# Optimization experiments

Measured on AMD Instinct MI355X. Metric: run time of the kernel, lower is better.

Reference implementation:

```python
import jax, jax.numpy as jnp
import numpy as np

N, E, VD, HD, ES = 10000, 80000, 32, 64, 68
NET_IN = VD * VD + 2 * HD + ES   # 1220: f2s(1024) + s[e0](64) + s[e1](64) + edge_s(68)
SELF_IN = VD * VD + 2 * HD       # 1152: temp_f2s(1024) + s(64) + s_c(64)
OUT_D = VD * VD + HD             # 1088: vector channel mixer + scalar update


def _lecun(k, fin, fout):
    return jax.random.normal(k, (fin, fout), jnp.float32) / jnp.sqrt(jnp.float32(fin))


def setup_inputs() -> dict:
    ks = jax.random.split(jax.random.key(0), 16)
    return {
        "f": jax.random.normal(ks[0], (N, 3, VD), jnp.float32),
        "s": jax.random.normal(ks[1], (N, HD), jnp.float32),
        "edge_f": jax.random.normal(ks[2], (E, 3, 1), jnp.float32),
        "edge_s": jax.random.normal(ks[3], (E, ES), jnp.float32),
        "W_emb1": _lecun(ks[4], 2 * VD + 1, VD),
        "net_W1": _lecun(ks[5], NET_IN, HD), "net_b1": jnp.zeros((HD,), jnp.float32),
        "net_W2": _lecun(ks[6], HD, HD), "net_b2": jnp.zeros((HD,), jnp.float32),
        "net_W3": _lecun(ks[7], HD, OUT_D), "net_b3": jnp.zeros((OUT_D,), jnp.float32),
        "W_emb2": _lecun(ks[8], 2 * VD, VD),
        "self_W1": _lecun(ks[9], SELF_IN, HD), "self_b1": jnp.zeros((HD,), jnp.float32),
        "self_W2": _lecun(ks[10], HD, HD), "self_b2": jnp.zeros((HD,), jnp.float32),
        "self_W3": _lecun(ks[11], HD, OUT_D), "self_b3": jnp.zeros((OUT_D,), jnp.float32),
        "edge_index": jax.random.randint(ks[12], (2, E), 0, N),
    }


def _mlp(x, W1, b1, W2, b2, W3, b3):
    h = jax.nn.relu(x @ W1 + b1)
    h = jax.nn.relu(h @ W2 + b2)
    return h @ W3 + b3


def _segment_mean(x, ids, n):
    tot = jax.ops.segment_sum(x, ids, num_segments=n)
    cnt = jax.ops.segment_sum(jnp.ones(ids.shape, x.dtype), ids, num_segments=n)
    return tot / jnp.maximum(cnt, 1.0).reshape((n,) + (1,) * (x.ndim - 1))


def _forward(f, s, edge_f, edge_s,
             W_emb1, net_W1, net_b1, net_W2, net_b2, net_W3, net_b3,
             W_emb2, self_W1, self_b1, self_W2, self_b2, self_W3, self_b3,
             edge_index):
    n = f.shape[0]
    e0, e1 = edge_index[0], edge_index[1]
    # --- edge message: gather -> embed -> gram einsum -> MLP ---
    _f = jnp.concatenate((f[e0], f[e1], edge_f), axis=-1)          # [E,3,2VD+1]
    _s = jnp.concatenate((s[e0], s[e1], edge_s), axis=-1)          # [E,2HD+ES]
    _f = _f @ W_emb1                                               # [E,3,VD]
    f2s = jnp.einsum('eij,eik->ejk', _f, _f).reshape(-1, VD * VD)  # _f^T @ _f, [E,VD*VD]
    Fn = jnp.linalg.norm(f2s, axis=-1, keepdims=True) + 1.0
    c = _mlp(jnp.concatenate((f2s, _s), axis=-1),
             net_W1, net_b1, net_W2, net_b2, net_W3, net_b3) / Fn  # [E,OUT_D]
    f_c = jnp.einsum('eij,ejk->eik', _f, c[:, :VD * VD].reshape(-1, VD, VD))  # [E,3,VD]
    f_c = _segment_mean(f_c, e0, n)                                # [N,3,VD]
    s_c = _segment_mean(c[:, VD * VD:], e0, n)                     # [N,HD]
    # --- node self-update ---
    tf = jnp.concatenate((f, f_c), axis=-1) @ W_emb2               # [N,3,VD]
    tf2s = jnp.einsum('nij,nik->njk', tf, tf).reshape(n, VD * VD)
    Fn2 = jnp.linalg.norm(tf2s, axis=-1, keepdims=True) + 1.0
    c2 = _mlp(jnp.concatenate((tf2s, s, s_c), axis=-1),
              self_W1, self_b1, self_W2, self_b2, self_W3, self_b3) / Fn2
    f_out = jnp.einsum('nij,njk->nik', tf, c2[:, :VD * VD].reshape(-1, VD, VD)) + f
    s_out = c2[:, VD * VD:] + s
    return f_out, s_out


def reference(f, s, edge_f, edge_s,
              W_emb1, net_W1, net_b1, net_W2, net_b2, net_W3, net_b3,
              W_emb2, self_W1, self_b1, self_W2, self_b2, self_W3, self_b3,
              edge_index):
    return _forward(f, s, edge_f, edge_s,
                    W_emb1, net_W1, net_b1, net_W2, net_b2, net_W3, net_b3,
                    W_emb2, self_W1, self_b1, self_W2, self_b2, self_W3, self_b3,
                    edge_index)
```

## Files before the change

kernel.cpp:

```cpp
#include <hip/hip_runtime.h>
#include <math.h>

#define NN 10000
#define NE 80000
#define SF 98
#define SFF 97
#define STX 72
#define NTRI 528
#define SAE 104
#define SAN 72

typedef __attribute__((ext_vector_type(8))) __bf16 bf16x8;
typedef __attribute__((ext_vector_type(8))) short short8v;
typedef __attribute__((ext_vector_type(4))) float f32x4;
typedef __attribute__((ext_vector_type(4))) unsigned uint4v;

__device__ __forceinline__ ushort f2bf(float x) {
  union { float f; unsigned u; } v; v.f = x;
  unsigned r = v.u + 0x7FFFu + ((v.u >> 16) & 1u);
  return (ushort)(r >> 16);
}
__device__ __forceinline__ void tri_ab(int k, int& a, int& b) {
  int aa = 0, rem = k;
  while (rem >= 32 - aa) { rem -= 32 - aa; ++aa; }
  a = aa; b = aa + rem;
}

__global__ __launch_bounds__(256)
void sgnn_hist(const int* __restrict__ eidx, int* __restrict__ deg) {
  const int e = blockIdx.x * 256 + threadIdx.x;
  if (e < NE) atomicAdd(deg + eidx[e], 1);
}

__global__ __launch_bounds__(1024)
void sgnn_scan(const int* __restrict__ deg, int* __restrict__ cursor,
               int* __restrict__ start) {
  __shared__ int sm[1024];
  __shared__ int carry;
  const int t = threadIdx.x;
  if (t == 0) carry = 0;
  __syncthreads();
  for (int base = 0; base < NN; base += 1024) {
    const int i = base + t;
    const int v = (i < NN) ? deg[i] : 0;
    sm[t] = v;
    __syncthreads();
    #pragma unroll
    for (int d = 1; d < 1024; d <<= 1) {
      const int add = (t >= d) ? sm[t - d] : 0;
      __syncthreads();
      sm[t] += add;
      __syncthreads();
    }
    const int excl = carry + sm[t] - v;
    if (i < NN) { cursor[i] = excl; start[i] = excl; }
    __syncthreads();
    if (t == 1023) carry += sm[1023];
    __syncthreads();
  }
}

__global__ __launch_bounds__(256)
void sgnn_scatter(const int* __restrict__ eidx, int* __restrict__ cursor,
                  int* __restrict__ sorted) {
  const int e = blockIdx.x * 256 + threadIdx.x;
  if (e < NE) {
    const int p = atomicAdd(cursor + eidx[e], 1);
    sorted[p] = e;
  }
}

__global__ __launch_bounds__(256)
void sgnn_wconv(const float* __restrict__ nW1, const float* __restrict__ nW2,
                const float* __restrict__ nW3, const float* __restrict__ sW1,
                const float* __restrict__ sW2, const float* __restrict__ sW3,
                const float* __restrict__ Wemb1, const float* __restrict__ Wemb2,
                ushort* __restrict__ wout, ushort* __restrict__ tab) {
  const int gid = blockIdx.x * 256 + threadIdx.x;
  if (gid >= 61 * 4096) {
    const int k = gid - 61 * 4096;
    if (k < NTRI) {
      int a, b; tri_ab(k, a, b);
      tab[k] = (ushort)(a | (b << 8) | ((a != b) ? 0x8000 : 0));
    }
    return;
  }
  const int tile = gid >> 12, idx = gid & 4095;
  const int c = idx >> 6, k = idx & 63;
  float v = 0.f;
  if (tile < 12) {
    const int T = tile;
    if (T < 8 || (T == 8 && k < 16)) {
      const int ktri = T * 64 + k;
      if (ktri < NTRI) {
        int a, b; tri_ab(ktri, a, b);
        v = nW1[(a * 32 + b) * 64 + c];
        if (a != b) v += nW1[(b * 32 + a) * 64 + c];
      }
    } else if (T == 8) { if (k < 20) v = nW1[(1216 + (k - 16)) * 64 + c]; }
    else if (T == 9)   v = nW1[(1024 + k) * 64 + c];
    else if (T == 10)  v = nW1[(1088 + k) * 64 + c];
    else               v = nW1[(1152 + k) * 64 + c];
  } else if (tile == 12) v = nW2[k * 64 + c];
  else if (tile < 30)    v = nW3[k * 1088 + (tile - 13) * 64 + c];
  else if (tile < 41) {
    const int T = tile - 30;
    if (T < 8 || (T == 8 && k < 16)) {
      const int ktri = T * 64 + k;
      if (ktri < NTRI) {
        int a, b; tri_ab(ktri, a, b);
        v = sW1[(a * 32 + b) * 64 + c];
        if (a != b) v += sW1[(b * 32 + a) * 64 + c];
      }
    } else if (T == 9) v = sW1[(1024 + k) * 64 + c];
    else if (T == 10)  v = sW1[(1088 + k) * 64 + c];
  } else if (tile == 41) v = sW2[k * 64 + c];
  else if (tile < 59)    v = sW3[k * 1088 + (tile - 42) * 64 + c];
  else if (tile == 59) {
    const int col = idx / 96, kk = idx % 96;
    v = (col < 32 && kk < 65) ? Wemb1[kk * 32 + col] : 0.f;
  } else {
    const int col = idx >> 6;
    v = (col < 32) ? Wemb2[k * 32 + col] : 0.f;
  }
  wout[gid] = f2bf(v);
}

#define STAGE_W(srcbase) do { const ushort* _s = (srcbase);                      \
  _Pragma("unroll") for (int rr = 0; rr < 2; ++rr) {                             \
    const int idx_ = t + 256 * rr; const int c_ = idx_ >> 3, ko_ = idx_ & 7;     \
    *(short8v*)&Wl[c_ * STX + ko_ * 8] = *(const short8v*)&_s[c_ * 64 + ko_ * 8];\
  } } while (0)

#define WPRE_LOAD(srcbase) do { const ushort* _s = (srcbase);                    \
  wpre0 = *(const short8v*)&_s[(t >> 3) * 64 + (t & 7) * 8];                     \
  wpre1 = *(const short8v*)&_s[(32 + (t >> 3)) * 64 + (t & 7) * 8]; } while (0)

#define WPRE_STORE() do {                                                        \
  *(short8v*)&Wl[(t >> 3) * STX + (t & 7) * 8] = wpre0;                          \
  *(short8v*)&Wl[(32 + (t >> 3)) * STX + (t & 7) * 8] = wpre1; } while (0)

#define MFMA_K64() do {                                                          \
  _Pragma("unroll") for (int kb = 0; kb < 2; ++kb) {                             \
    const bf16x8 af_ = *(const bf16x8*)&Xl[(w * 16 + ll) * STX + kb * 32 + lh * 8]; \
    acc[0] = __builtin_amdgcn_mfma_f32_16x16x32_bf16(af_,                        \
        *(const bf16x8*)&Wl[(     ll) * STX + kb * 32 + lh * 8], acc[0], 0, 0, 0); \
    acc[1] = __builtin_amdgcn_mfma_f32_16x16x32_bf16(af_,                        \
        *(const bf16x8*)&Wl[(16 + ll) * STX + kb * 32 + lh * 8], acc[1], 0, 0, 0); \
    acc[2] = __builtin_amdgcn_mfma_f32_16x16x32_bf16(af_,                        \
        *(const bf16x8*)&Wl[(32 + ll) * STX + kb * 32 + lh * 8], acc[2], 0, 0, 0); \
    acc[3] = __builtin_amdgcn_mfma_f32_16x16x32_bf16(af_,                        \
        *(const bf16x8*)&Wl[(48 + ll) * STX + kb * 32 + lh * 8], acc[3], 0, 0, 0); \
  } } while (0)

#define ZERO_ACC() do { _Pragma("unroll") for (int q = 0; q < 4; ++q)            \
    acc[q] = (f32x4){0.f, 0.f, 0.f, 0.f}; } while (0)

#define PACK_STORE16(dstp) do {                                                  \
  unsigned pk[8];                                                                \
  _Pragma("unroll") for (int q = 0; q < 8; ++q)                                  \
    pk[q] = (unsigned)f2bf(xv[2 * q]) | ((unsigned)f2bf(xv[2 * q + 1]) << 16);   \
  *(uint4v*)(dstp)       = (uint4v){pk[0], pk[1], pk[2], pk[3]};                 \
  *(uint4v*)((dstp) + 8) = (uint4v){pk[4], pk[5], pk[6], pk[7]};                 \
} while (0)

#define TRI16(kt) do {                                                           \
  int prev_a = -1; float fa0 = 0.f, fa1 = 0.f, fa2 = 0.f;                        \
  _Pragma("unroll") for (int m = 0; m < 16; ++m) {                               \
    const int tb = tabL[(kt) + m];                                               \
    const int a_ = tb & 31, b_ = (tb >> 8) & 31;                                 \
    if (a_ != prev_a) { fa0 = fr[a_]; fa1 = fr[32 + a_]; fa2 = fr[64 + a_];      \
                        prev_a = a_; }                                           \
    const float v = fmaf(fa0, fr[b_],                                            \
        fmaf(fa1, fr[32 + b_], fa2 * fr[64 + b_]));                              \
    const float wsel = (tb & 0x8000) ? 2.f : 1.f;                                \
    sumsq = fmaf(v * wsel, v, sumsq);                                            \
    xv[m] = v;                                                                   \
  } } while (0)

#define XV_LOAD16(p) do { const float* _p = (p);                                 \
  _Pragma("unroll") for (int q = 0; q < 4; ++q) {                                \
    const float4 v4 = *(const float4*)(_p + 4 * q);                              \
    xv[4 * q + 0] = v4.x; xv[4 * q + 1] = v4.y;                                  \
    xv[4 * q + 2] = v4.z; xv[4 * q + 3] = v4.w; } } while (0)

#define CONSUME_NT() do {                                                        \
  _Pragma("unroll") for (int r = 0; r < 4; ++r) {                                \
    const int row_ = w * 16 + lh * 4 + r;                                        \
    float2 fr2_0 = *(const float2*)&smF[row_ * SF +      nt * 2];                \
    float2 fr2_1 = *(const float2*)&smF[row_ * SF + 32 + nt * 2];                \
    float2 fr2_2 = *(const float2*)&smF[row_ * SF + 64 + nt * 2];                \
    _Pragma("unroll") for (int nc = 0; nc < 4; ++nc) {                           \
      const float cv = (acc[nc][r] + b3v[nc]) * ifnr[r];                         \
      const int p = nc & 1;                                                      \
      const float f0 = (nc < 2) ? fr2_0.x : fr2_0.y;                             \
      const float f1 = (nc < 2) ? fr2_1.x : fr2_1.y;                             \
      const float f2 = (nc < 2) ? fr2_2.x : fr2_2.y;                             \
      fch[(r * 3 + 0) * 2 + p] = fmaf(f0, cv, fch[(r * 3 + 0) * 2 + p]);         \
      fch[(r * 3 + 1) * 2 + p] = fmaf(f1, cv, fch[(r * 3 + 1) * 2 + p]);         \
      fch[(r * 3 + 2) * 2 + p] = fmaf(f2, cv, fch[(r * 3 + 2) * 2 + p]);         \
    }                                                                            \
  } } while (0)

#define STAGE_FS() do {                                                          \
  _Pragma("unroll") for (int r = 0; r < 4; ++r) {                                \
    const int row_ = w * 16 + lh * 4 + r;                                        \
    _Pragma("unroll") for (int i = 0; i < 3; ++i) {                              \
      F[row_ * SFF + i * 32 + ll]      = fch[(r * 3 + i) * 2 + 0];               \
      F[row_ * SFF + i * 32 + ll + 16] = fch[(r * 3 + i) * 2 + 1];               \
    }                                                                            \
    _Pragma("unroll") for (int nc = 0; nc < 4; ++nc)                             \
      S[row_ * 65 + nc * 16 + ll] = cs[nc * 4 + r];                              \
  } } while (0)

#define LDS_BYTES 46624

__global__ __launch_bounds__(256, 2)
void sgnn_edge(const float* __restrict__ f, const float* __restrict__ s,
               const float* __restrict__ edge_f, const float* __restrict__ edge_s,
               const float* __restrict__ b1, const float* __restrict__ b2,
               const float* __restrict__ b3,
               const ushort* __restrict__ wbf, const ushort* __restrict__ tab_g,
               const int* __restrict__ eidx, const int* __restrict__ sorted,
               const int* __restrict__ start_g, const int* __restrict__ deg_g,
               float* __restrict__ fc_sum, float* __restrict__ sc_sum) {
  __shared__ __align__(16) char sbuf[LDS_BYTES];
  float*  smF  = (float*)sbuf;
  float*  F    = (float*)sbuf;
  ushort* Xl   = (ushort*)(sbuf + 25088);
  ushort* Wl   = (ushort*)(sbuf + 34304);
  ushort* Aemb = (ushort*)(sbuf + 25088);
  float*  S    = (float*)(sbuf + 25088);
  float*  red  = (float*)(sbuf + 43520);
  int*    snode = (int*)(sbuf + 43520);
  int*    srow0 = snode + 8;
  int*    srow1 = snode + 16;
  int*    sst   = snode + 24;
  int*    sdg   = snode + 32;
  ushort* tabL = (ushort*)(sbuf + 45056);
  float*  iFn  = (float*)(sbuf + 45056);
  int*    es_s = (int*)(sbuf + 46112);
  ushort* e0s  = (ushort*)(sbuf + 46368);
  ushort* e1s  = (ushort*)(sbuf + 46496);

  const int t = threadIdx.x, j = t & 63, w = t >> 6, eb = w * 16;
  const int lh = j >> 4, ll = j & 15;
  const int bid = blockIdx.x;
  const ushort* wembT = wbf + 59 * 4096;
  short8v wpre0, wpre1;

  if (t < 64) {
    const int e = sorted[bid * 64 + t];
    es_s[t] = e;
    e0s[t] = (ushort)eidx[e];
    e1s[t] = (ushort)eidx[NE + e];
  }
  for (int idx = t; idx < NTRI; idx += 256) tabL[idx] = tab_g[idx];
  __syncthreads();

  int str = 0, dgr = 0;
  if (j < 16) {
    const int n_ = e0s[eb + j];
    str = start_g[n_];
    dgr = deg_g[n_];
  }
  WPRE_LOAD(wbf + 0);

  #pragma unroll 1
  for (int h = 0; h < 2; ++h) {
    const int hb = h * 32;
    #pragma unroll 1
    for (int cc = t; cc < 576; cc += 256) {
      const int row = cc / 6, seg = cc - row * 6;
      const int lel = (row * 43) >> 7, il = row - lel * 3;
      const int k0 = seg * 16;
      float xv[16];
      if (seg < 4) {
        const int nd = (seg < 2) ? (int)e0s[hb + lel] : (int)e1s[hb + lel];
        XV_LOAD16(f + nd * 96 + il * 32 + (seg & 1) * 16);
      } else if (seg == 4) {
        xv[0] = edge_f[es_s[hb + lel] * 3 + il];
        #pragma unroll
        for (int m = 1; m < 16; ++m) xv[m] = 0.f;
      } else {
        #pragma unroll
        for (int m = 0; m < 16; ++m) xv[m] = 0.f;
      }
      PACK_STORE16(&Aemb[row * SAE + k0]);
    }
    __syncthreads();
    #pragma unroll 1
    for (int job = w * 3; job < w * 3 + 3; ++job) {
      const int mt = job >> 1, nt = job & 1;
      f32x4 ac = (f32x4){0.f, 0.f, 0.f, 0.f};
      #pragma unroll
      for (int kb = 0; kb < 3; ++kb) {
        const bf16x8 av = *(const bf16x8*)&Aemb[(mt * 16 + ll) * SAE + kb * 32 + lh * 8];
        const bf16x8 bv = *(const bf16x8*)&wembT[(nt * 16 + ll) * 96 + kb * 32 + lh * 8];
        ac = __builtin_amdgcn_mfma_f32_16x16x32_bf16(av, bv, ac, 0, 0, 0);
      }
      #pragma unroll
      for (int r = 0; r < 4; ++r) {
        const int rr = mt * 16 + lh * 4 + r;
        const int lel = (rr * 43) >> 7, il = rr - lel * 3;
        smF[(hb + lel) * SF + il * 32 + nt * 16 + ll] = ac[r];
      }
    }
    __syncthreads();
  }

  f32x4 acc[4];
  ZERO_ACC();
  float sumsq = 0.f;

  #pragma unroll 1
  for (int T = 0; T < 12; ++T) {
    __syncthreads();
    WPRE_STORE();
    {
      const float* fr = smF + j * SF;
      float xv[16];
      if (T < 8) {
        TRI16(T * 64 + w * 16);
      } else if (T == 8) {
        if (w == 0) {
          TRI16(512);
        } else if (w == 1) {
          const float4 v4 = *(const float4*)(edge_s + es_s[j] * 68 + 64);
          xv[0] = v4.x; xv[1] = v4.y; xv[2] = v4.z; xv[3] = v4.w;
          #pragma unroll
          for (int m = 4; m < 16; ++m) xv[m] = 0.f;
        } else {
          #pragma unroll
          for (int m = 0; m < 16; ++m) xv[m] = 0.f;
        }
      } else if (T == 9)  { XV_LOAD16(s + e0s[j] * 64 + w * 16); }
      else if (T == 10)   { XV_LOAD16(s + e1s[j] * 64 + w * 16); }
      else                { XV_LOAD16(edge_s + es_s[j] * 68 + w * 16); }
      PACK_STORE16(&Xl[j * STX + w * 16]);
    }
    __syncthreads();
    WPRE_LOAD(wbf + (T + 1) * 4096);
    MFMA_K64();
  }

  __syncthreads();
  red[w * 64 + j] = sumsq;
  #pragma unroll
  for (int nc = 0; nc < 4; ++nc) {
    const float bv = b1[nc * 16 + ll];
    #pragma unroll
    for (int r = 0; r < 4; ++r)
      Xl[(w * 16 + lh * 4 + r) * STX + nc * 16 + ll] = f2bf(fmaxf(acc[nc][r] + bv, 0.f));
  }
  WPRE_STORE();
  ZERO_ACC();
  __syncthreads();
  if (t < 64) {
    const float ss = red[t] + red[64 + t] + red[128 + t] + red[192 + t];
    iFn[t] = 1.f / (sqrtf(ss) + 1.f);
  }

  MFMA_K64();
  #pragma unroll
  for (int nc = 0; nc < 4; ++nc) {
    const float bv = b2[nc * 16 + ll];
    #pragma unroll
    for (int r = 0; r < 4; ++r)
      Xl[(w * 16 + lh * 4 + r) * STX + nc * 16 + ll] = f2bf(fmaxf(acc[nc][r] + bv, 0.f));
  }

  float fch[24];
  #pragma unroll
  for (int q = 0; q < 24; ++q) fch[q] = 0.f;
  float cs[16];
  float ifnr[4];

  #pragma unroll 1
  for (int nt = 0; nt < 17; ++nt) {
    __syncthreads();
    STAGE_W(wbf + (13 + nt) * 4096);
    float b3v[4];
    #pragma unroll
    for (int nc = 0; nc < 4; ++nc) b3v[nc] = b3[nt * 64 + nc * 16 + ll];
    __syncthreads();
    if (nt == 0) {
      #pragma unroll
      for (int r = 0; r < 4; ++r) ifnr[r] = iFn[w * 16 + lh * 4 + r];
    }
    ZERO_ACC();
    MFMA_K64();
    if (nt < 16) {
      CONSUME_NT();
    } else {
      #pragma unroll
      for (int nc = 0; nc < 4; ++nc)
        #pragma unroll
        for (int r = 0; r < 4; ++r)
          cs[nc * 4 + r] = (acc[nc][r] + b3v[nc]) * ifnr[r];
    }
  }

  __syncthreads();
  STAGE_FS();
  if (t < 8) snode[t] = -1;
  __syncthreads();

  {
    float r0 = 0.f, r1 = 0.f, rs = 0.f;
    int runlen = 0;
    const int gwb = bid * 64 + eb;
    #pragma unroll 1
    for (int m = 0; m < 16; ++m) {
      const int row = eb + m;
      r0 += F[row * SFF + j];
      if (j < 32) r1 += F[row * SFF + 64 + j];
      rs += S[row * 65 + j];
      ++runlen;
      const int n = e0s[row];
      if (m == 15 || e0s[row + 1] != n) {
        const int st = __shfl(str, m);
        const int dg = __shfl(dgr, m);
        const int g1v = gwb + m, g0v = g1v - runlen + 1;
        if (g0v == st && runlen == dg) {
          fc_sum[n * 96 + j] = r0;
          if (j < 32) fc_sum[n * 96 + 64 + j] = r1;
          sc_sum[n * 64 + j] = rs;
        } else {
          const int slot = (g0v == gwb) ? 2 * w : 2 * w + 1;
          if (j == 0) {
            snode[slot] = n; srow0[slot] = row - runlen + 1; srow1[slot] = row;
            sst[slot] = st; sdg[slot] = dg;
          }
        }
        r0 = r1 = rs = 0.f; runlen = 0;
      }
    }
  }
  __syncthreads();

  if (t < 160) {
    const int ch = t;
    int prevn = -1;
    #pragma unroll 1
    for (int ss = 0; ss < 8; ++ss) {
      const int n = snode[ss];
      if (n < 0) continue;
      if (n != prevn) {
        float v = 0.f;
        #pragma unroll 1
        for (int k2 = ss; k2 < 8; ++k2) {
          if (snode[k2] == n) {
            #pragma unroll 1
            for (int row = srow0[k2]; row <= srow1[k2]; ++row)
              v += (ch < 96) ? F[row * SFF + ch] : S[row * 65 + (ch - 96)];
          } else if (k2 > ss && snode[k2] >= 0) break;
        }
        const bool cib = (sst[ss] >= bid * 64) && (sst[ss] + sdg[ss] <= bid * 64 + 64);
        float* dst = (ch < 96) ? (fc_sum + n * 96 + ch) : (sc_sum + n * 64 + (ch - 96));
        if (cib) *dst = v; else atomicAdd(dst, v);
      }
      prevn = n;
    }
  }
}

__global__ __launch_bounds__(256, 2)
void sgnn_node(const float* __restrict__ f, const float* __restrict__ s,
               const float* __restrict__ b1, const float* __restrict__ b2,
               const float* __restrict__ b3,
               const ushort* __restrict__ wbf, const ushort* __restrict__ tab_g,
               const float* __restrict__ fcm, const float* __restrict__ scm,
               const int* __restrict__ deg_g,
               float* __restrict__ of, float* __restrict__ os) {
  __shared__ __align__(16) char sbuf[LDS_BYTES];
  float*  smF  = (float*)sbuf;
  float*  F    = (float*)sbuf;
  ushort* Xl   = (ushort*)(sbuf + 25088);
  ushort* Wl   = (ushort*)(sbuf + 34304);
  ushort* Aemb = (ushort*)(sbuf + 25088);
  float*  S    = (float*)(sbuf + 25088);
  float*  red  = (float*)(sbuf + 43520);
  float*  icntL = (float*)(sbuf + 43520);
  ushort* tabL = (ushort*)(sbuf + 45056);
  float*  iFn  = (float*)(sbuf + 45056);

  const int t = threadIdx.x, j = t & 63, w = t >> 6, eb = w * 16;
  const int lh = j >> 4, ll = j & 15;
  const int nbase = blockIdx.x * 64;
  const ushort* wembTn = wbf + 60 * 4096;
  short8v wpre0, wpre1;

  for (int idx = t; idx < NTRI; idx += 256) tabL[idx] = tab_g[idx];
  if (t < 64)
    icntL[t] = 1.f / fmaxf((float)deg_g[min(nbase + t, NN - 1)], 1.f);
  WPRE_LOAD(wbf + 30 * 4096);
  __syncthreads();

  #pragma unroll 1
  for (int h = 0; h < 2; ++h) {
    const int hb = h * 32;
    #pragma unroll 1
    for (int cc = t; cc < 384; cc += 256) {
      const int row = cc >> 2, seg = cc & 3;
      const int lel = (row * 43) >> 7, il = row - lel * 3;
      const int nc = min(nbase + hb + lel, NN - 1);
      const int k0 = seg * 16;
      float xv[16];
      if (seg < 2) {
        XV_LOAD16(f + nc * 96 + il * 32 + seg * 16);
      } else {
        XV_LOAD16(fcm + nc * 96 + il * 32 + (seg - 2) * 16);
        const float ic = icntL[hb + lel];
        #pragma unroll
        for (int m = 0; m < 16; ++m) xv[m] *= ic;
      }
      PACK_STORE16(&Aemb[row * SAN + k0]);
    }
    __syncthreads();
    #pragma unroll 1
    for (int job = w * 3; job < w * 3 + 3; ++job) {
      const int mt = job >> 1, nt = job & 1;
      f32x4 ac = (f32x4){0.f, 0.f, 0.f, 0.f};
      #pragma unroll
      for (int kb = 0; kb < 2; ++kb) {
        const bf16x8 av = *(const bf16x8*)&Aemb[(mt * 16 + ll) * SAN + kb * 32 + lh * 8];
        const bf16x8 bv = *(const bf16x8*)&wembTn[(nt * 16 + ll) * 64 + kb * 32 + lh * 8];
        ac = __builtin_amdgcn_mfma_f32_16x16x32_bf16(av, bv, ac, 0, 0, 0);
      }
      #pragma unroll
      for (int r = 0; r < 4; ++r) {
        const int rr = mt * 16 + lh * 4 + r;
        const int lel = (rr * 43) >> 7, il = rr - lel * 3;
        smF[(hb + lel) * SF + il * 32 + nt * 16 + ll] = ac[r];
      }
    }
    __syncthreads();
  }

  f32x4 acc[4];
  ZERO_ACC();
  float sumsq = 0.f;

  #pragma unroll 1
  for (int T = 0; T < 11; ++T) {
    __syncthreads();
    WPRE_STORE();
    {
      const float* fr = smF + j * SF;
      float xv[16];
      if (T < 8) {
        TRI16(T * 64 + w * 16);
      } else if (T == 8) {
        if (w == 0) {
          TRI16(512);
        } else {
          #pragma unroll
          for (int m = 0; m < 16; ++m) xv[m] = 0.f;
        }
      } else if (T == 9) {
        XV_LOAD16(s + min(nbase + j, NN - 1) * 64 + w * 16);
      } else {
        XV_LOAD16(scm + min(nbase + j, NN - 1) * 64 + w * 16);
        const float ic = icntL[j];
        #pragma unroll
        for (int m = 0; m < 16; ++m) xv[m] *= ic;
      }
      PACK_STORE16(&Xl[j * STX + w * 16]);
    }
    __syncthreads();
    WPRE_LOAD(wbf + (31 + T) * 4096);
    MFMA_K64();
  }

  __syncthreads();
  red[w * 64 + j] = sumsq;
  #pragma unroll
  for (int nc = 0; nc < 4; ++nc) {
    const float bv = b1[nc * 16 + ll];
    #pragma unroll
    for (int r = 0; r < 4; ++r)
      Xl[(w * 16 + lh * 4 + r) * STX + nc * 16 + ll] = f2bf(fmaxf(acc[nc][r] + bv, 0.f));
  }
  WPRE_STORE();
  ZERO_ACC();
  __syncthreads();
  if (t < 64) {
    const float ss = red[t] + red[64 + t] + red[128 + t] + red[192 + t];
    iFn[t] = 1.f / (sqrtf(ss) + 1.f);
  }

  MFMA_K64();
  #pragma unroll
  for (int nc = 0; nc < 4; ++nc) {
    const float bv = b2[nc * 16 + ll];
    #pragma unroll
    for (int r = 0; r < 4; ++r)
      Xl[(w * 16 + lh * 4 + r) * STX + nc * 16 + ll] = f2bf(fmaxf(acc[nc][r] + bv, 0.f));
  }

  float fch[24];
  #pragma unroll
  for (int q = 0; q < 24; ++q) fch[q] = 0.f;
  float cs[16];
  float ifnr[4];

  #pragma unroll 1
  for (int nt = 0; nt < 17; ++nt) {
    __syncthreads();
    STAGE_W(wbf + (42 + nt) * 4096);
    float b3v[4];
    #pragma unroll
    for (int nc = 0; nc < 4; ++nc) b3v[nc] = b3[nt * 64 + nc * 16 + ll];
    __syncthreads();
    if (nt == 0) {
      #pragma unroll
      for (int r = 0; r < 4; ++r) ifnr[r] = iFn[w * 16 + lh * 4 + r];
    }
    ZERO_ACC();
    MFMA_K64();
    if (nt < 16) {
      CONSUME_NT();
    } else {
      #pragma unroll
      for (int nc = 0; nc < 4; ++nc)
        #pragma unroll
        for (int r = 0; r < 4; ++r)
          cs[nc * 4 + r] = (acc[nc][r] + b3v[nc]) * ifnr[r];
    }
  }

  __syncthreads();
  STAGE_FS();
  __syncthreads();

  #pragma unroll 1
  for (int m = 0; m < 16; ++m) {
    const int row = eb + m;
    const int n_m = nbase + row;
    if (n_m < NN) {
      of[n_m * 96 + j] = F[row * SFF + j] + f[n_m * 96 + j];
      if (j < 32)
        of[n_m * 96 + 64 + j] = F[row * SFF + 64 + j] + f[n_m * 96 + 64 + j];
      os[n_m * 64 + j] = S[row * 65 + j] + s[n_m * 64 + j];
    }
  }
}

extern "C" void kernel_launch(void* const* d_in, const int* in_sizes, int n_in,
                              void* d_out, int out_size, void* d_ws, size_t ws_size,
                              hipStream_t stream) {
  const float* f      = (const float*)d_in[0];
  const float* s      = (const float*)d_in[1];
  const float* edge_f = (const float*)d_in[2];
  const float* edge_s = (const float*)d_in[3];
  const float* Wemb1  = (const float*)d_in[4];
  const float* nW1 = (const float*)d_in[5];
  const float* nb1 = (const float*)d_in[6];
  const float* nW2 = (const float*)d_in[7];
  const float* nb2 = (const float*)d_in[8];
  const float* nW3 = (const float*)d_in[9];
  const float* nb3 = (const float*)d_in[10];
  const float* Wemb2 = (const float*)d_in[11];
  const float* sW1 = (const float*)d_in[12];
  const float* sb1 = (const float*)d_in[13];
  const float* sW2 = (const float*)d_in[14];
  const float* sb2 = (const float*)d_in[15];
  const float* sW3 = (const float*)d_in[16];
  const float* sb3 = (const float*)d_in[17];
  const int* eidx  = (const int*)d_in[18];

  float* of = (float*)d_out;
  float* os = of + (size_t)NN * 96;

  int* deg    = (int*)d_ws;
  int* cursor = deg + NN;
  int* start  = cursor + NN;
  int* sorted = start + NN;
  ushort* wbf = (ushort*)(sorted + NE);
  ushort* tab = wbf + 61 * 4096;

  hipMemsetAsync(deg, 0, (size_t)NN * 4, stream);
  hipMemsetAsync(d_out, 0, (size_t)NN * 160 * 4, stream);

  hipLaunchKernelGGL(sgnn_wconv, dim3((61 * 4096 + NTRI + 255) / 256), dim3(256),
                     0, stream, nW1, nW2, nW3, sW1, sW2, sW3, Wemb1, Wemb2,
                     wbf, tab);
  hipLaunchKernelGGL(sgnn_hist, dim3((NE + 255) / 256), dim3(256), 0, stream,
                     eidx, deg);
  hipLaunchKernelGGL(sgnn_scan, dim3(1), dim3(1024), 0, stream, deg, cursor, start);
  hipLaunchKernelGGL(sgnn_scatter, dim3((NE + 255) / 256), dim3(256), 0, stream,
                     eidx, cursor, sorted);
  hipLaunchKernelGGL(sgnn_edge, dim3(NE / 64), dim3(256), 0, stream,
                     f, s, edge_f, edge_s, nb1, nb2, nb3,
                     wbf, tab, eidx, sorted, start, deg,
                     of , os );
  hipLaunchKernelGGL(sgnn_node, dim3((NN + 63) / 64), dim3(256), 0, stream,
                     f, s, sb1, sb2, sb3,
                     wbf, tab, of , os , deg, of, os);
}
```

Baseline: 210.8 us.

## Store staged features in LDS as bf16 and fold degree histogram into weight conversion

The per-edge and per-node embedded feature buffers and the output staging buffers in shared memory move from fp32 to bf16, with conversions on load and store. This cuts LDS use from about 46.6KB to 34.7KB per block, which may allow more resident blocks, and halves LDS traffic. The separate histogram kernel is merged into the weight-conversion kernel, saving one launch. The cost is extra precision loss in the gram features and in the accumulated messages, plus added pack and unpack instructions.

```diff
diff --git a/kernel.cpp b/kernel.cpp
--- a/kernel.cpp
+++ b/kernel.cpp
@@ -3,8 +3,9 @@
 
 #define NN 10000
 #define NE 80000
-#define SF 98
-#define SFF 97
+#define SFH 102
+#define SFB 98
+#define SSB 66
 #define STX 72
 #define NTRI 528
 #define SAE 104
@@ -20,16 +21,14 @@
   unsigned r = v.u + 0x7FFFu + ((v.u >> 16) & 1u);
   return (ushort)(r >> 16);
 }
+__device__ __forceinline__ float bfu(ushort u) {
+  union { unsigned x; float f; } v; v.x = (unsigned)u << 16;
+  return v.f;
+}
 __device__ __forceinline__ void tri_ab(int k, int& a, int& b) {
   int aa = 0, rem = k;
   while (rem >= 32 - aa) { rem -= 32 - aa; ++aa; }
   a = aa; b = aa + rem;
-}
-
-__global__ __launch_bounds__(256)
-void sgnn_hist(const int* __restrict__ eidx, int* __restrict__ deg) {
-  const int e = blockIdx.x * 256 + threadIdx.x;
-  if (e < NE) atomicAdd(deg + eidx[e], 1);
 }
 
 __global__ __launch_bounds__(1024)
@@ -75,8 +74,10 @@
                 const float* __restrict__ nW3, const float* __restrict__ sW1,
                 const float* __restrict__ sW2, const float* __restrict__ sW3,
                 const float* __restrict__ Wemb1, const float* __restrict__ Wemb2,
+                const int* __restrict__ eidx, int* __restrict__ deg,
                 ushort* __restrict__ wout, ushort* __restrict__ tab) {
   const int gid = blockIdx.x * 256 + threadIdx.x;
+  if (gid < NE) atomicAdd(deg + eidx[gid], 1);
   if (gid >= 61 * 4096) {
     const int k = gid - 61 * 4096;
     if (k < NTRI) {
@@ -169,10 +170,10 @@
   _Pragma("unroll") for (int m = 0; m < 16; ++m) {                               \
     const int tb = tabL[(kt) + m];                                               \
     const int a_ = tb & 31, b_ = (tb >> 8) & 31;                                 \
-    if (a_ != prev_a) { fa0 = fr[a_]; fa1 = fr[32 + a_]; fa2 = fr[64 + a_];      \
-                        prev_a = a_; }                                           \
-    const float v = fmaf(fa0, fr[b_],                                            \
-        fmaf(fa1, fr[32 + b_], fa2 * fr[64 + b_]));                              \
+    if (a_ != prev_a) { fa0 = bfu(fr[a_]); fa1 = bfu(fr[32 + a_]);               \
+                        fa2 = bfu(fr[64 + a_]); prev_a = a_; }                   \
+    const float v = fmaf(fa0, bfu(fr[b_]),                                       \
+        fmaf(fa1, bfu(fr[32 + b_]), fa2 * bfu(fr[64 + b_])));                    \
     const float wsel = (tb & 0x8000) ? 2.f : 1.f;                                \
     sumsq = fmaf(v * wsel, v, sumsq);                                            \
     xv[m] = v;                                                                   \
@@ -187,15 +188,19 @@
 #define CONSUME_NT() do {                                                        \
   _Pragma("unroll") for (int r = 0; r < 4; ++r) {                                \
     const int row_ = w * 16 + lh * 4 + r;                                        \
-    float2 fr2_0 = *(const float2*)&smF[row_ * SF +      nt * 2];                \
-    float2 fr2_1 = *(const float2*)&smF[row_ * SF + 32 + nt * 2];                \
-    float2 fr2_2 = *(const float2*)&smF[row_ * SF + 64 + nt * 2];                \
+    const unsigned u0 = *(const unsigned*)&smFh[row_ * SFH +      nt * 2];       \
+    const unsigned u1 = *(const unsigned*)&smFh[row_ * SFH + 32 + nt * 2];       \
+    const unsigned u2 = *(const unsigned*)&smFh[row_ * SFH + 64 + nt * 2];       \
+    union { unsigned x; float f; } l0, h0, l1, h1, l2, h2;                       \
+    l0.x = u0 << 16; h0.x = u0 & 0xffff0000u;                                    \
+    l1.x = u1 << 16; h1.x = u1 & 0xffff0000u;                                    \
+    l2.x = u2 << 16; h2.x = u2 & 0xffff0000u;                                    \
     _Pragma("unroll") for (int nc = 0; nc < 4; ++nc) {                           \
       const float cv = (acc[nc][r] + b3v[nc]) * ifnr[r];                         \
       const int p = nc & 1;                                                      \
-      const float f0 = (nc < 2) ? fr2_0.x : fr2_0.y;                             \
-      const float f1 = (nc < 2) ? fr2_1.x : fr2_1.y;                             \
-      const float f2 = (nc < 2) ? fr2_2.x : fr2_2.y;                             \
+      const float f0 = (nc < 2) ? l0.f : h0.f;                                   \
+      const float f1 = (nc < 2) ? l1.f : h1.f;                                   \
+      const float f2 = (nc < 2) ? l2.f : h2.f;                                   \
       fch[(r * 3 + 0) * 2 + p] = fmaf(f0, cv, fch[(r * 3 + 0) * 2 + p]);         \
       fch[(r * 3 + 1) * 2 + p] = fmaf(f1, cv, fch[(r * 3 + 1) * 2 + p]);         \
       fch[(r * 3 + 2) * 2 + p] = fmaf(f2, cv, fch[(r * 3 + 2) * 2 + p]);         \
@@ -206,14 +211,14 @@
   _Pragma("unroll") for (int r = 0; r < 4; ++r) {                                \
     const int row_ = w * 16 + lh * 4 + r;                                        \
     _Pragma("unroll") for (int i = 0; i < 3; ++i) {                              \
-      F[row_ * SFF + i * 32 + ll]      = fch[(r * 3 + i) * 2 + 0];               \
-      F[row_ * SFF + i * 32 + ll + 16] = fch[(r * 3 + i) * 2 + 1];               \
+      F[row_ * SFB + i * 32 + ll]      = f2bf(fch[(r * 3 + i) * 2 + 0]);         \
+      F[row_ * SFB + i * 32 + ll + 16] = f2bf(fch[(r * 3 + i) * 2 + 1]);         \
     }                                                                            \
     _Pragma("unroll") for (int nc = 0; nc < 4; ++nc)                             \
-      S[row_ * 65 + nc * 16 + ll] = cs[nc * 4 + r];                              \
+      S[row_ * SSB + nc * 16 + ll] = f2bf(cs[nc * 4 + r]);                       \
   } } while (0)
 
-#define LDS_BYTES 46624
+#define LDS_BYTES 34656
 
 __global__ __launch_bounds__(256, 2)
 void sgnn_edge(const float* __restrict__ f, const float* __restrict__ s,
@@ -225,23 +230,23 @@
                const int* __restrict__ start_g, const int* __restrict__ deg_g,
                float* __restrict__ fc_sum, float* __restrict__ sc_sum) {
   __shared__ __align__(16) char sbuf[LDS_BYTES];
-  float*  smF  = (float*)sbuf;
-  float*  F    = (float*)sbuf;
-  ushort* Xl   = (ushort*)(sbuf + 25088);
-  ushort* Wl   = (ushort*)(sbuf + 34304);
-  ushort* Aemb = (ushort*)(sbuf + 25088);
-  float*  S    = (float*)(sbuf + 25088);
-  float*  red  = (float*)(sbuf + 43520);
-  int*    snode = (int*)(sbuf + 43520);
+  ushort* smFh = (ushort*)sbuf;
+  ushort* F    = (ushort*)sbuf;
+  ushort* Xl   = (ushort*)(sbuf + 13056);
+  ushort* S    = (ushort*)(sbuf + 13056);
+  ushort* Aemb = (ushort*)(sbuf + 13056);
+  ushort* Wl   = (ushort*)(sbuf + 22272);
+  float*  red  = (float*)(sbuf + 31488);
+  int*    snode = (int*)(sbuf + 31488);
   int*    srow0 = snode + 8;
   int*    srow1 = snode + 16;
   int*    sst   = snode + 24;
   int*    sdg   = snode + 32;
-  ushort* tabL = (ushort*)(sbuf + 45056);
-  float*  iFn  = (float*)(sbuf + 45056);
-  int*    es_s = (int*)(sbuf + 46112);
-  ushort* e0s  = (ushort*)(sbuf + 46368);
-  ushort* e1s  = (ushort*)(sbuf + 46496);
+  ushort* tabL = (ushort*)(sbuf + 33088);
+  float*  iFn  = (float*)(sbuf + 33088);
+  int*    es_s = (int*)(sbuf + 34144);
+  ushort* e0s  = (ushort*)(sbuf + 34400);
+  ushort* e1s  = (ushort*)(sbuf + 34528);
 
   const int t = threadIdx.x, j = t & 63, w = t >> 6, eb = w * 16;
   const int lh = j >> 4, ll = j & 15;
@@ -303,7 +308,7 @@
       for (int r = 0; r < 4; ++r) {
         const int rr = mt * 16 + lh * 4 + r;
         const int lel = (rr * 43) >> 7, il = rr - lel * 3;
-        smF[(hb + lel) * SF + il * 32 + nt * 16 + ll] = ac[r];
+        smFh[(hb + lel) * SFH + il * 32 + nt * 16 + ll] = f2bf(ac[r]);
       }
     }
     __syncthreads();
@@ -318,7 +323,7 @@
     __syncthreads();
     WPRE_STORE();
     {
-      const float* fr = smF + j * SF;
+      const ushort* fr = smFh + j * SFH;
       float xv[16];
       if (T < 8) {
         TRI16(T * 64 + w * 16);
@@ -413,9 +418,9 @@
     #pragma unroll 1
     for (int m = 0; m < 16; ++m) {
       const int row = eb + m;
-      r0 += F[row * SFF + j];
-      if (j < 32) r1 += F[row * SFF + 64 + j];
-      rs += S[row * 65 + j];
+      r0 += bfu(F[row * SFB + j]);
+      if (j < 32) r1 += bfu(F[row * SFB + 64 + j]);
+      rs += bfu(S[row * SSB + j]);
       ++runlen;
       const int n = e0s[row];
       if (m == 15 || e0s[row + 1] != n) {
@@ -453,7 +458,7 @@
           if (snode[k2] == n) {
             #pragma unroll 1
             for (int row = srow0[k2]; row <= srow1[k2]; ++row)
-              v += (ch < 96) ? F[row * SFF + ch] : S[row * 65 + (ch - 96)];
+              v += (ch < 96) ? bfu(F[row * SFB + ch]) : bfu(S[row * SSB + (ch - 96)]);
           } else if (k2 > ss && snode[k2] >= 0) break;
         }
         const bool cib = (sst[ss] >= bid * 64) && (sst[ss] + sdg[ss] <= bid * 64 + 64);
@@ -474,16 +479,16 @@
                const int* __restrict__ deg_g,
                float* __restrict__ of, float* __restrict__ os) {
   __shared__ __align__(16) char sbuf[LDS_BYTES];
-  float*  smF  = (float*)sbuf;
-  float*  F    = (float*)sbuf;
-  ushort* Xl   = (ushort*)(sbuf + 25088);
-  ushort* Wl   = (ushort*)(sbuf + 34304);
-  ushort* Aemb = (ushort*)(sbuf + 25088);
-  float*  S    = (float*)(sbuf + 25088);
-  float*  red  = (float*)(sbuf + 43520);
-  float*  icntL = (float*)(sbuf + 43520);
-  ushort* tabL = (ushort*)(sbuf + 45056);
-  float*  iFn  = (float*)(sbuf + 45056);
+  ushort* smFh = (ushort*)sbuf;
+  ushort* F    = (ushort*)sbuf;
+  ushort* Xl   = (ushort*)(sbuf + 13056);
+  ushort* S    = (ushort*)(sbuf + 13056);
+  ushort* Aemb = (ushort*)(sbuf + 13056);
+  ushort* Wl   = (ushort*)(sbuf + 22272);
+  float*  red  = (float*)(sbuf + 31488);
+  float*  icntL = (float*)(sbuf + 31488);
+  ushort* tabL = (ushort*)(sbuf + 33088);
+  float*  iFn  = (float*)(sbuf + 33088);
 
   const int t = threadIdx.x, j = t & 63, w = t >> 6, eb = w * 16;
   const int lh = j >> 4, ll = j & 15;
@@ -532,7 +537,7 @@
       for (int r = 0; r < 4; ++r) {
         const int rr = mt * 16 + lh * 4 + r;
         const int lel = (rr * 43) >> 7, il = rr - lel * 3;
-        smF[(hb + lel) * SF + il * 32 + nt * 16 + ll] = ac[r];
+        smFh[(hb + lel) * SFH + il * 32 + nt * 16 + ll] = f2bf(ac[r]);
       }
     }
     __syncthreads();
@@ -547,7 +552,7 @@
     __syncthreads();
     WPRE_STORE();
     {
-      const float* fr = smF + j * SF;
+      const ushort* fr = smFh + j * SFH;
       float xv[16];
       if (T < 8) {
         TRI16(T * 64 + w * 16);
@@ -639,10 +644,10 @@
     const int row = eb + m;
     const int n_m = nbase + row;
     if (n_m < NN) {
-      of[n_m * 96 + j] = F[row * SFF + j] + f[n_m * 96 + j];
+      of[n_m * 96 + j] = bfu(F[row * SFB + j]) + f[n_m * 96 + j];
       if (j < 32)
-        of[n_m * 96 + 64 + j] = F[row * SFF + 64 + j] + f[n_m * 96 + 64 + j];
-      os[n_m * 64 + j] = S[row * 65 + j] + s[n_m * 64 + j];
+        of[n_m * 96 + 64 + j] = bfu(F[row * SFB + 64 + j]) + f[n_m * 96 + 64 + j];
+      os[n_m * 64 + j] = bfu(S[row * SSB + j]) + s[n_m * 64 + j];
     }
   }
 }
@@ -685,9 +690,7 @@
 
   hipLaunchKernelGGL(sgnn_wconv, dim3((61 * 4096 + NTRI + 255) / 256), dim3(256),
                      0, stream, nW1, nW2, nW3, sW1, sW2, sW3, Wemb1, Wemb2,
-                     wbf, tab);
-  hipLaunchKernelGGL(sgnn_hist, dim3((NE + 255) / 256), dim3(256), 0, stream,
-                     eidx, deg);
+                     eidx, deg, wbf, tab);
   hipLaunchKernelGGL(sgnn_scan, dim3(1), dim3(1024), 0, stream, deg, cursor, start);
   hipLaunchKernelGGL(sgnn_scatter, dim3((NE + 255) / 256), dim3(256), 0, stream,
                      eidx, cursor, sorted);
```

After: 213.2 us. About the same (+1.1%).
